# Kernel tuning notes

Measured on AMD Instinct MI355X. Metric: run time of the kernel, lower is better.

Reference implementation:

```python
import jax, jax.numpy as jnp
import numpy as np

B, LQ, LK, D = 4, 256, 256, 768


def setup_inputs() -> dict:
    key = jax.random.key(0)
    ks = jax.random.split(key, 11)
    s = 1.0 / np.sqrt(D)
    return {
        "query": jax.random.normal(ks[0], (B, LQ, D), jnp.float32),
        "key": jax.random.normal(ks[1], (B, LK, D), jnp.float32),
        "value": jax.random.normal(ks[2], (B, LK, D), jnp.float32),
        "Wq": jax.random.uniform(ks[3], (D, D), jnp.float32, -s, s),
        "bq": jax.random.uniform(ks[4], (D,), jnp.float32, -s, s),
        "Wk": jax.random.uniform(ks[5], (D, D), jnp.float32, -s, s),
        "bk": jax.random.uniform(ks[6], (D,), jnp.float32, -s, s),
        "Wv": jax.random.uniform(ks[7], (D, D), jnp.float32, -s, s),
        "bv": jax.random.uniform(ks[8], (D,), jnp.float32, -s, s),
        "Ws": jax.random.uniform(ks[9], (D,), jnp.float32, -s, s),
        "bs": jax.random.uniform(ks[10], (), jnp.float32, -s, s),
    }


def reference(query, key, value, Wq, bq, Wk, bk, Wv, bv, Ws, bs):
    # Linear projections (torch Linear: x @ W.T + b; here W stored as [in, out])
    q = jnp.einsum('bqd,de->bqe', query, Wq) + bq   # [B,Lq,D]
    k = jnp.einsum('bkd,de->bke', key, Wk) + bk     # [B,Lk,D]
    v = jnp.einsum('bkd,de->bke', value, Wv) + bv   # [B,Lk,D]
    # Additive (Bahdanau) scores: tanh(q_i + k_j) . Ws + bs  -> [B,Lq,Lk]
    h = jnp.tanh(q[:, :, None, :] + k[:, None, :, :])  # [B,Lq,Lk,D]
    scores = jnp.einsum('bqkd,d->bqk', h, Ws) + bs
    attention_weights = jax.nn.softmax(scores, axis=-1)  # [B,Lq,Lk]
    attended = jnp.einsum('bqk,bkd->bqd', attention_weights, v)
    return attended, attention_weights
```

## Files before the change

### kernel.cpp

```cpp
#include <hip/hip_runtime.h>

#define NB 4
#define SLQ 256
#define SLK 256
#define DD 768

#define TWO_LOG2E 2.8853900817779268f
#define LOG2E 1.4426950408889634f

typedef _Float16 f16x4 __attribute__((ext_vector_type(4)));
typedef _Float16 f16x8 __attribute__((ext_vector_type(8)));
typedef float f32x4 __attribute__((ext_vector_type(4)));

__device__ __forceinline__ float fexp2(float x) { return __builtin_amdgcn_exp2f(x); }
__device__ __forceinline__ float frcp(float x) { return __builtin_amdgcn_rcpf(x); }

#define LSTR 40

__global__ __launch_bounds__(256) void qkv_f16_kernel(
    const float* __restrict__ query, const float* __restrict__ key_in,
    const float* __restrict__ value, const float* __restrict__ Wq,
    const float* __restrict__ bq, const float* __restrict__ Wk,
    const float* __restrict__ bk, const float* __restrict__ Wv,
    const float* __restrict__ bv, float* __restrict__ eq,
    _Float16* __restrict__ ekh, _Float16* __restrict__ vsh)
{
    const int z = blockIdx.z;
    const float* A = (z == 0) ? query : (z == 1) ? key_in : value;
    const float* W = (z == 0) ? Wq : (z == 1) ? Wk : Wv;
    const float* bias = (z == 0) ? bq : (z == 1) ? bk : bv;

    __shared__ _Float16 Ah[64 * LSTR];
    __shared__ _Float16 Bt[64 * LSTR];

    const int tid = threadIdx.x;
    const int lane = tid & 63;
    const int wid = tid >> 6;
    const int wr = wid >> 1;
    const int wc = wid & 1;
    const int row0 = blockIdx.y * 64;
    const int col0 = blockIdx.x * 64;

    const int ar = tid >> 3;
    const int ac4 = (tid & 7) << 2;
    const int bk_ = tid >> 4;
    const int bn4 = (tid & 15) << 2;

    float4 pa0, pa1, pb0, pb1;
    {
        pa0 = *(const float4*)&A[(size_t)(row0 + ar) * DD + ac4];
        pa1 = *(const float4*)&A[(size_t)(row0 + ar + 32) * DD + ac4];
        pb0 = *(const float4*)&W[(size_t)bk_ * DD + col0 + bn4];
        pb1 = *(const float4*)&W[(size_t)(bk_ + 16) * DD + col0 + bn4];
    }

    f32x4 acc[2][2] = {};
    const int kj = (lane >> 4) << 3;
    const int fr = lane & 15;

    for (int s = 0; s < DD / 32; ++s) {
        __syncthreads();
        {
            f16x4 h;
            h[0] = (_Float16)pa0.x; h[1] = (_Float16)pa0.y;
            h[2] = (_Float16)pa0.z; h[3] = (_Float16)pa0.w;
            *(f16x4*)&Ah[ar * LSTR + ac4] = h;
            h[0] = (_Float16)pa1.x; h[1] = (_Float16)pa1.y;
            h[2] = (_Float16)pa1.z; h[3] = (_Float16)pa1.w;
            *(f16x4*)&Ah[(ar + 32) * LSTR + ac4] = h;
            Bt[(bn4 + 0) * LSTR + bk_] = (_Float16)pb0.x;
            Bt[(bn4 + 1) * LSTR + bk_] = (_Float16)pb0.y;
            Bt[(bn4 + 2) * LSTR + bk_] = (_Float16)pb0.z;
            Bt[(bn4 + 3) * LSTR + bk_] = (_Float16)pb0.w;
            Bt[(bn4 + 0) * LSTR + bk_ + 16] = (_Float16)pb1.x;
            Bt[(bn4 + 1) * LSTR + bk_ + 16] = (_Float16)pb1.y;
            Bt[(bn4 + 2) * LSTR + bk_ + 16] = (_Float16)pb1.z;
            Bt[(bn4 + 3) * LSTR + bk_ + 16] = (_Float16)pb1.w;
        }
        __syncthreads();
        if (s + 1 < DD / 32) {
            const int ks = (s + 1) * 32;
            pa0 = *(const float4*)&A[(size_t)(row0 + ar) * DD + ks + ac4];
            pa1 = *(const float4*)&A[(size_t)(row0 + ar + 32) * DD + ks + ac4];
            pb0 = *(const float4*)&W[(size_t)(ks + bk_) * DD + col0 + bn4];
            pb1 = *(const float4*)&W[(size_t)(ks + bk_ + 16) * DD + col0 + bn4];
        }
        f16x8 af0 = *(const f16x8*)&Ah[(wr * 32 + fr) * LSTR + kj];
        f16x8 af1 = *(const f16x8*)&Ah[(wr * 32 + 16 + fr) * LSTR + kj];
        f16x8 bf0 = *(const f16x8*)&Bt[(wc * 32 + fr) * LSTR + kj];
        f16x8 bf1 = *(const f16x8*)&Bt[(wc * 32 + 16 + fr) * LSTR + kj];
        acc[0][0] = __builtin_amdgcn_mfma_f32_16x16x32_f16(af0, bf0, acc[0][0], 0, 0, 0);
        acc[0][1] = __builtin_amdgcn_mfma_f32_16x16x32_f16(af0, bf1, acc[0][1], 0, 0, 0);
        acc[1][0] = __builtin_amdgcn_mfma_f32_16x16x32_f16(af1, bf0, acc[1][0], 0, 0, 0);
        acc[1][1] = __builtin_amdgcn_mfma_f32_16x16x32_f16(af1, bf1, acc[1][1], 0, 0, 0);
    }

    const int colb = col0 + wc * 32 + fr;
    const int rowb = row0 + wr * 32 + ((lane >> 4) << 2);
#pragma unroll
    for (int mf = 0; mf < 2; ++mf) {
#pragma unroll
        for (int nf = 0; nf < 2; ++nf) {
            const int col = colb + nf * 16;
            const float bv = bias[col];
#pragma unroll
            for (int r = 0; r < 4; ++r) {
                const int row = rowb + mf * 16 + r;
                const float val = acc[mf][nf][r] + bv;
                if (z == 0) {
                    eq[(size_t)row * DD + col] = fexp2(fminf(val * TWO_LOG2E, 15.0f));
                } else if (z == 1) {
                    ekh[(size_t)row * DD + col] =
                        (_Float16)fexp2(fminf(val * TWO_LOG2E, 15.0f));
                } else {
                    vsh[(size_t)row * DD + col] = (_Float16)val;
                }
            }
        }
    }
}

__global__ __launch_bounds__(256) void scores_kernel(
    const float* __restrict__ Eq, const _Float16* __restrict__ Ekh,
    const float* __restrict__ Ws, float* __restrict__ logits)
{
    const int b = blockIdx.z;
    const int k0 = blockIdx.x * 64;
    const int q0 = blockIdx.y * 8;
    const int lane = threadIdx.x & 63;
    const int wid = __builtin_amdgcn_readfirstlane((int)(threadIdx.x >> 6));
    const int q = q0 + (wid << 1);

    const _Float16* kr = Ekh + (size_t)(b * SLK + k0 + lane) * DD;
    const float* qp0 = Eq + (size_t)(b * SLQ + q) * DD;
    const float* qp1 = qp0 + DD;

    float acc0 = 0.f, acc1 = 0.f;

    f16x4 e[4], en[4];
    float g0[16], g1[16], w[16], g0n[16], g1n[16], wn[16];
#pragma unroll
    for (int j = 0; j < 4; ++j) e[j] = *(const f16x4*)(kr + j * 4);
#pragma unroll
    for (int j = 0; j < 16; ++j) { g0[j] = qp0[j]; g1[j] = qp1[j]; w[j] = Ws[j]; }

    for (int c = 0; c < DD / 16; ++c) {
        const int dn = (c + 1) * 16;
        if (c + 1 < DD / 16) {
#pragma unroll
            for (int j = 0; j < 4; ++j) en[j] = *(const f16x4*)(kr + dn + j * 4);
#pragma unroll
            for (int j = 0; j < 16; ++j) {
                g0n[j] = qp0[dn + j]; g1n[j] = qp1[dn + j]; wn[j] = Ws[dn + j];
            }
        }
#pragma unroll
        for (int j = 0; j < 16; ++j) {
            const float ev = (float)e[j >> 2][j & 3];
            const float r0 = frcp(fmaf(g0[j], ev, 1.0f));
            const float r1 = frcp(fmaf(g1[j], ev, 1.0f));
            acc0 = fmaf(w[j], r0, acc0);
            acc1 = fmaf(w[j], r1, acc1);
        }
#pragma unroll
        for (int j = 0; j < 4; ++j) e[j] = en[j];
#pragma unroll
        for (int j = 0; j < 16; ++j) { g0[j] = g0n[j]; g1[j] = g1n[j]; w[j] = wn[j]; }
    }

    logits[(size_t)(b * SLQ + q) * SLK + k0 + lane] = -2.0f * acc0;
    logits[(size_t)(b * SLQ + q + 1) * SLK + k0 + lane] = -2.0f * acc1;
}

__global__ __launch_bounds__(256) void softmax_kernel(float* __restrict__ attn,
                                                      _Float16* __restrict__ phalf)
{
    const int lane = threadIdx.x & 63;
    const int wave = threadIdx.x >> 6;
    const int row = blockIdx.x * 4 + wave;
    float* rp = attn + (size_t)row * SLK;

    float4 x = *(const float4*)&rp[lane << 2];
    float m = fmaxf(fmaxf(x.x, x.y), fmaxf(x.z, x.w));
#pragma unroll
    for (int off = 32; off; off >>= 1) m = fmaxf(m, __shfl_xor(m, off, 64));

    float e0 = fexp2((x.x - m) * LOG2E);
    float e1 = fexp2((x.y - m) * LOG2E);
    float e2 = fexp2((x.z - m) * LOG2E);
    float e3 = fexp2((x.w - m) * LOG2E);
    float s = (e0 + e1) + (e2 + e3);
#pragma unroll
    for (int off = 32; off; off >>= 1) s += __shfl_xor(s, off, 64);

    const float inv = 1.0f / s;
    float4 o;
    o.x = e0 * inv; o.y = e1 * inv; o.z = e2 * inv; o.w = e3 * inv;
    *(float4*)&rp[lane << 2] = o;

    f16x4 h;
    h[0] = (_Float16)o.x; h[1] = (_Float16)o.y;
    h[2] = (_Float16)o.z; h[3] = (_Float16)o.w;
    *(f16x4*)&phalf[(size_t)row * SLK + (lane << 2)] = h;
}

__global__ __launch_bounds__(256) void attended_f16_kernel(
    const _Float16* __restrict__ phalf, const _Float16* __restrict__ vsh,
    float* __restrict__ out)
{
    const int b = blockIdx.z;
    const _Float16* P = phalf + (size_t)b * SLQ * SLK;
    const _Float16* V = vsh + (size_t)b * SLK * DD;
    float* C = out + (size_t)b * SLQ * DD;

    __shared__ _Float16 Ah[64 * LSTR];
    __shared__ _Float16 Bt[64 * LSTR];

    const int tid = threadIdx.x;
    const int lane = tid & 63;
    const int wid = tid >> 6;
    const int wr = wid >> 1;
    const int wc = wid & 1;
    const int row0 = blockIdx.y * 64;
    const int col0 = blockIdx.x * 64;

    const int ar = tid >> 2;
    const int ac8 = (tid & 3) << 3;
    const int bk_ = tid >> 3;
    const int bn8 = (tid & 7) << 3;

    f16x8 pa = *(const f16x8*)&P[(size_t)(row0 + ar) * SLK + ac8];
    f16x8 pb = *(const f16x8*)&V[(size_t)bk_ * DD + col0 + bn8];

    f32x4 acc[2][2] = {};
    const int kj = (lane >> 4) << 3;
    const int fr = lane & 15;

    for (int s = 0; s < SLK / 32; ++s) {
        __syncthreads();
        *(f16x8*)&Ah[ar * LSTR + ac8] = pa;
#pragma unroll
        for (int i = 0; i < 8; ++i) Bt[(bn8 + i) * LSTR + bk_] = pb[i];
        __syncthreads();
        if (s + 1 < SLK / 32) {
            const int ks = (s + 1) * 32;
            pa = *(const f16x8*)&P[(size_t)(row0 + ar) * SLK + ks + ac8];
            pb = *(const f16x8*)&V[(size_t)(ks + bk_) * DD + col0 + bn8];
        }
        f16x8 af0 = *(const f16x8*)&Ah[(wr * 32 + fr) * LSTR + kj];
        f16x8 af1 = *(const f16x8*)&Ah[(wr * 32 + 16 + fr) * LSTR + kj];
        f16x8 bf0 = *(const f16x8*)&Bt[(wc * 32 + fr) * LSTR + kj];
        f16x8 bf1 = *(const f16x8*)&Bt[(wc * 32 + 16 + fr) * LSTR + kj];
        acc[0][0] = __builtin_amdgcn_mfma_f32_16x16x32_f16(af0, bf0, acc[0][0], 0, 0, 0);
        acc[0][1] = __builtin_amdgcn_mfma_f32_16x16x32_f16(af0, bf1, acc[0][1], 0, 0, 0);
        acc[1][0] = __builtin_amdgcn_mfma_f32_16x16x32_f16(af1, bf0, acc[1][0], 0, 0, 0);
        acc[1][1] = __builtin_amdgcn_mfma_f32_16x16x32_f16(af1, bf1, acc[1][1], 0, 0, 0);
    }

    const int colb = col0 + wc * 32 + fr;
    const int rowb = row0 + wr * 32 + ((lane >> 4) << 2);
#pragma unroll
    for (int mf = 0; mf < 2; ++mf)
#pragma unroll
        for (int nf = 0; nf < 2; ++nf)
#pragma unroll
            for (int r = 0; r < 4; ++r)
                C[(size_t)(rowb + mf * 16 + r) * DD + colb + nf * 16] = acc[mf][nf][r];
}

extern "C" void kernel_launch(void* const* d_in, const int* in_sizes, int n_in,
                              void* d_out, int out_size, void* d_ws, size_t ws_size,
                              hipStream_t stream)
{
    (void)in_sizes; (void)n_in; (void)out_size; (void)ws_size;

    const float* query = (const float*)d_in[0];
    const float* key   = (const float*)d_in[1];
    const float* value = (const float*)d_in[2];
    const float* Wq = (const float*)d_in[3];
    const float* bq = (const float*)d_in[4];
    const float* Wk = (const float*)d_in[5];
    const float* bk = (const float*)d_in[6];
    const float* Wv = (const float*)d_in[7];
    const float* bv = (const float*)d_in[8];
    const float* Ws = (const float*)d_in[9];

    const size_t NE = (size_t)NB * SLQ * DD;
    float* eq = (float*)d_ws;
    _Float16* ekh = (_Float16*)(eq + NE);
    _Float16* vsh = ekh + NE;
    _Float16* phalf = vsh + NE;

    float* out = (float*)d_out;
    float* attended = out;
    float* attnw = out + NE;

    qkv_f16_kernel<<<dim3(DD / 64, (NB * SLQ) / 64, 3), 256, 0, stream>>>(
        query, key, value, Wq, bq, Wk, bk, Wv, bv, eq, ekh, vsh);
    scores_kernel<<<dim3(SLK / 64, SLQ / 8, NB), 256, 0, stream>>>(eq, ekh, Ws, attnw);
    softmax_kernel<<<dim3((NB * SLQ) / 4), 256, 0, stream>>>(attnw, phalf);
    attended_f16_kernel<<<dim3(DD / 64, SLQ / 64, NB), 256, 0, stream>>>(phalf, vsh, attended);
}
```

Measured before the change: 157.8 us.

## Pre-convert inputs to fp16, transpose weights/V, fuse scores with softmax

Adds prep kernels that convert Q/K/V activations to fp16 and transpose the projection weights to fp16 [out,in], so the QKV GEMM loads vectorized fp16 rows and skips per-element LDS transposes. V is written transposed so the attended GEMM also loads contiguous rows. Scores and softmax are fused into one kernel with one query row per block, so the fp32 logits are no longer written and reread. This adds two extra launches and extra workspace traffic. The scores kernel now computes one query per thread instead of two, which loses reuse of the K loads.

Result: slower. 174.9 us (+10.8%).

```diff
diff --git a/kernel.cpp b/kernel.cpp
--- a/kernel.cpp
+++ b/kernel.cpp
@@ -17,21 +17,71 @@
 
 #define LSTR 40
 
+__global__ __launch_bounds__(256) void prep_a_kernel(
+    const float* __restrict__ q, const float* __restrict__ k,
+    const float* __restrict__ v, _Float16* __restrict__ qh,
+    _Float16* __restrict__ kh, _Float16* __restrict__ vh)
+{
+    const int z = blockIdx.z;
+    const float* src = (z == 0) ? q : (z == 1) ? k : v;
+    _Float16* dst = (z == 0) ? qh : (z == 1) ? kh : vh;
+    const int i8 = (blockIdx.x * 256 + threadIdx.x) * 8;
+    float4 a = *(const float4*)&src[i8];
+    float4 b = *(const float4*)&src[i8 + 4];
+    f16x8 h;
+    h[0] = (_Float16)a.x; h[1] = (_Float16)a.y; h[2] = (_Float16)a.z; h[3] = (_Float16)a.w;
+    h[4] = (_Float16)b.x; h[5] = (_Float16)b.y; h[6] = (_Float16)b.z; h[7] = (_Float16)b.w;
+    *(f16x8*)&dst[i8] = h;
+}
+
+__global__ __launch_bounds__(256) void prep_wt_kernel(
+    const float* __restrict__ Wq, const float* __restrict__ Wk,
+    const float* __restrict__ Wv, _Float16* __restrict__ wtq,
+    _Float16* __restrict__ wtk, _Float16* __restrict__ wtv)
+{
+    const int z = blockIdx.z;
+    const float* W = (z == 0) ? Wq : (z == 1) ? Wk : Wv;
+    _Float16* Wt = (z == 0) ? wtq : (z == 1) ? wtk : wtv;
+
+    __shared__ float t[64][65];
+    const int tid = threadIdx.x;
+    const int kt0 = blockIdx.y * 64;
+    const int nt0 = blockIdx.x * 64;
+
+    const int col4 = (tid & 15) << 2;
+#pragma unroll
+    for (int i = 0; i < 4; ++i) {
+        const int row = ((tid >> 4) << 2) + i;
+        *(float4*)&t[row][col4] = *(const float4*)&W[(size_t)(kt0 + row) * DD + nt0 + col4];
+    }
+    __syncthreads();
+    const int n = tid >> 2;
+    const int k16 = (tid & 3) << 4;
+    f16x8 h0, h1;
+#pragma unroll
+    for (int j = 0; j < 8; ++j) {
+        h0[j] = (_Float16)t[k16 + j][n];
+        h1[j] = (_Float16)t[k16 + 8 + j][n];
+    }
+    *(f16x8*)&Wt[(size_t)(nt0 + n) * DD + kt0 + k16] = h0;
+    *(f16x8*)&Wt[(size_t)(nt0 + n) * DD + kt0 + k16 + 8] = h1;
+}
+
 __global__ __launch_bounds__(256) void qkv_f16_kernel(
-    const float* __restrict__ query, const float* __restrict__ key_in,
-    const float* __restrict__ value, const float* __restrict__ Wq,
-    const float* __restrict__ bq, const float* __restrict__ Wk,
-    const float* __restrict__ bk, const float* __restrict__ Wv,
+    const _Float16* __restrict__ qh, const _Float16* __restrict__ kh,
+    const _Float16* __restrict__ vh, const _Float16* __restrict__ wtq,
+    const _Float16* __restrict__ wtk, const _Float16* __restrict__ wtv,
+    const float* __restrict__ bq, const float* __restrict__ bk,
     const float* __restrict__ bv, float* __restrict__ eq,
-    _Float16* __restrict__ ekh, _Float16* __restrict__ vsh)
+    _Float16* __restrict__ ekh, _Float16* __restrict__ vsht)
 {
     const int z = blockIdx.z;
-    const float* A = (z == 0) ? query : (z == 1) ? key_in : value;
-    const float* W = (z == 0) ? Wq : (z == 1) ? Wk : Wv;
+    const _Float16* A = (z == 0) ? qh : (z == 1) ? kh : vh;
+    const _Float16* Wt = (z == 0) ? wtq : (z == 1) ? wtk : wtv;
     const float* bias = (z == 0) ? bq : (z == 1) ? bk : bv;
 
     __shared__ _Float16 Ah[64 * LSTR];
-    __shared__ _Float16 Bt[64 * LSTR];
+    __shared__ _Float16 Bh[64 * LSTR];
 
     const int tid = threadIdx.x;
     const int lane = tid & 63;
@@ -41,18 +91,14 @@
     const int row0 = blockIdx.y * 64;
     const int col0 = blockIdx.x * 64;
 
-    const int ar = tid >> 3;
-    const int ac4 = (tid & 7) << 2;
-    const int bk_ = tid >> 4;
-    const int bn4 = (tid & 15) << 2;
-
-    float4 pa0, pa1, pb0, pb1;
-    {
-        pa0 = *(const float4*)&A[(size_t)(row0 + ar) * DD + ac4];
-        pa1 = *(const float4*)&A[(size_t)(row0 + ar + 32) * DD + ac4];
-        pb0 = *(const float4*)&W[(size_t)bk_ * DD + col0 + bn4];
-        pb1 = *(const float4*)&W[(size_t)(bk_ + 16) * DD + col0 + bn4];
-    }
+    const int sr = tid >> 2;
+    const int sc = (tid & 3) << 3;
+
+    const _Float16* Ap = A + (size_t)(row0 + sr) * DD + sc;
+    const _Float16* Bp = Wt + (size_t)(col0 + sr) * DD + sc;
+
+    f16x8 pa = *(const f16x8*)Ap;
+    f16x8 pb = *(const f16x8*)Bp;
 
     f32x4 acc[2][2] = {};
     const int kj = (lane >> 4) << 3;
@@ -60,35 +106,17 @@
 
     for (int s = 0; s < DD / 32; ++s) {
         __syncthreads();
-        {
-            f16x4 h;
-            h[0] = (_Float16)pa0.x; h[1] = (_Float16)pa0.y;
-            h[2] = (_Float16)pa0.z; h[3] = (_Float16)pa0.w;
-            *(f16x4*)&Ah[ar * LSTR + ac4] = h;
-            h[0] = (_Float16)pa1.x; h[1] = (_Float16)pa1.y;
-            h[2] = (_Float16)pa1.z; h[3] = (_Float16)pa1.w;
-            *(f16x4*)&Ah[(ar + 32) * LSTR + ac4] = h;
-            Bt[(bn4 + 0) * LSTR + bk_] = (_Float16)pb0.x;
-            Bt[(bn4 + 1) * LSTR + bk_] = (_Float16)pb0.y;
-            Bt[(bn4 + 2) * LSTR + bk_] = (_Float16)pb0.z;
-            Bt[(bn4 + 3) * LSTR + bk_] = (_Float16)pb0.w;
-            Bt[(bn4 + 0) * LSTR + bk_ + 16] = (_Float16)pb1.x;
-            Bt[(bn4 + 1) * LSTR + bk_ + 16] = (_Float16)pb1.y;
-            Bt[(bn4 + 2) * LSTR + bk_ + 16] = (_Float16)pb1.z;
-            Bt[(bn4 + 3) * LSTR + bk_ + 16] = (_Float16)pb1.w;
-        }
+        *(f16x8*)&Ah[sr * LSTR + sc] = pa;
+        *(f16x8*)&Bh[sr * LSTR + sc] = pb;
         __syncthreads();
         if (s + 1 < DD / 32) {
-            const int ks = (s + 1) * 32;
-            pa0 = *(const float4*)&A[(size_t)(row0 + ar) * DD + ks + ac4];
-            pa1 = *(const float4*)&A[(size_t)(row0 + ar + 32) * DD + ks + ac4];
-            pb0 = *(const float4*)&W[(size_t)(ks + bk_) * DD + col0 + bn4];
-            pb1 = *(const float4*)&W[(size_t)(ks + bk_ + 16) * DD + col0 + bn4];
+            pa = *(const f16x8*)(Ap + (s + 1) * 32);
+            pb = *(const f16x8*)(Bp + (s + 1) * 32);
         }
         f16x8 af0 = *(const f16x8*)&Ah[(wr * 32 + fr) * LSTR + kj];
         f16x8 af1 = *(const f16x8*)&Ah[(wr * 32 + 16 + fr) * LSTR + kj];
-        f16x8 bf0 = *(const f16x8*)&Bt[(wc * 32 + fr) * LSTR + kj];
-        f16x8 bf1 = *(const f16x8*)&Bt[(wc * 32 + 16 + fr) * LSTR + kj];
+        f16x8 bf0 = *(const f16x8*)&Bh[(wc * 32 + fr) * LSTR + kj];
+        f16x8 bf1 = *(const f16x8*)&Bh[(wc * 32 + 16 + fr) * LSTR + kj];
         acc[0][0] = __builtin_amdgcn_mfma_f32_16x16x32_f16(af0, bf0, acc[0][0], 0, 0, 0);
         acc[0][1] = __builtin_amdgcn_mfma_f32_16x16x32_f16(af0, bf1, acc[0][1], 0, 0, 0);
         acc[1][0] = __builtin_amdgcn_mfma_f32_16x16x32_f16(af1, bf0, acc[1][0], 0, 0, 0);
@@ -102,119 +130,103 @@
 #pragma unroll
         for (int nf = 0; nf < 2; ++nf) {
             const int col = colb + nf * 16;
-            const float bv = bias[col];
+            const float bvv = bias[col];
 #pragma unroll
             for (int r = 0; r < 4; ++r) {
                 const int row = rowb + mf * 16 + r;
-                const float val = acc[mf][nf][r] + bv;
+                const float val = acc[mf][nf][r] + bvv;
                 if (z == 0) {
                     eq[(size_t)row * DD + col] = fexp2(fminf(val * TWO_LOG2E, 15.0f));
                 } else if (z == 1) {
                     ekh[(size_t)row * DD + col] =
                         (_Float16)fexp2(fminf(val * TWO_LOG2E, 15.0f));
                 } else {
-                    vsh[(size_t)row * DD + col] = (_Float16)val;
+                    vsht[((size_t)(row >> 8) * DD + col) * SLK + (row & 255)] =
+                        (_Float16)val;
                 }
             }
         }
     }
 }
 
-__global__ __launch_bounds__(256) void scores_kernel(
+__global__ __launch_bounds__(256) void scores_softmax_kernel(
     const float* __restrict__ Eq, const _Float16* __restrict__ Ekh,
-    const float* __restrict__ Ws, float* __restrict__ logits)
-{
-    const int b = blockIdx.z;
-    const int k0 = blockIdx.x * 64;
-    const int q0 = blockIdx.y * 8;
-    const int lane = threadIdx.x & 63;
-    const int wid = __builtin_amdgcn_readfirstlane((int)(threadIdx.x >> 6));
-    const int q = q0 + (wid << 1);
-
-    const _Float16* kr = Ekh + (size_t)(b * SLK + k0 + lane) * DD;
-    const float* qp0 = Eq + (size_t)(b * SLQ + q) * DD;
-    const float* qp1 = qp0 + DD;
-
-    float acc0 = 0.f, acc1 = 0.f;
-
-    f16x4 e[4], en[4];
-    float g0[16], g1[16], w[16], g0n[16], g1n[16], wn[16];
-#pragma unroll
-    for (int j = 0; j < 4; ++j) e[j] = *(const f16x4*)(kr + j * 4);
-#pragma unroll
-    for (int j = 0; j < 16; ++j) { g0[j] = qp0[j]; g1[j] = qp1[j]; w[j] = Ws[j]; }
+    const float* __restrict__ Ws, float* __restrict__ attnw,
+    _Float16* __restrict__ phalf)
+{
+    const int qrow = blockIdx.x;
+    const int b = blockIdx.y;
+    const int tid = threadIdx.x;
+    const int lane = tid & 63;
+    const int w = tid >> 6;
+
+    const _Float16* kr = Ekh + (size_t)(b * SLK + tid) * DD;
+    const float* qp = Eq + (size_t)(b * SLQ + qrow) * DD;
+
+    float acc0 = 0.f, acc1 = 0.f, acc2 = 0.f, acc3 = 0.f;
+
+    f16x8 e0 = *(const f16x8*)kr;
+    f16x8 e1 = *(const f16x8*)(kr + 8);
+    float g[16], wv[16], gn[16], wn[16];
+#pragma unroll
+    for (int j = 0; j < 16; ++j) { g[j] = qp[j]; wv[j] = Ws[j]; }
 
     for (int c = 0; c < DD / 16; ++c) {
+        f16x8 en0, en1;
         const int dn = (c + 1) * 16;
         if (c + 1 < DD / 16) {
-#pragma unroll
-            for (int j = 0; j < 4; ++j) en[j] = *(const f16x4*)(kr + dn + j * 4);
-#pragma unroll
-            for (int j = 0; j < 16; ++j) {
-                g0n[j] = qp0[dn + j]; g1n[j] = qp1[dn + j]; wn[j] = Ws[dn + j];
-            }
-        }
-#pragma unroll
-        for (int j = 0; j < 16; ++j) {
-            const float ev = (float)e[j >> 2][j & 3];
-            const float r0 = frcp(fmaf(g0[j], ev, 1.0f));
-            const float r1 = frcp(fmaf(g1[j], ev, 1.0f));
-            acc0 = fmaf(w[j], r0, acc0);
-            acc1 = fmaf(w[j], r1, acc1);
-        }
-#pragma unroll
-        for (int j = 0; j < 4; ++j) e[j] = en[j];
-#pragma unroll
-        for (int j = 0; j < 16; ++j) { g0[j] = g0n[j]; g1[j] = g1n[j]; w[j] = wn[j]; }
-    }
-
-    logits[(size_t)(b * SLQ + q) * SLK + k0 + lane] = -2.0f * acc0;
-    logits[(size_t)(b * SLQ + q + 1) * SLK + k0 + lane] = -2.0f * acc1;
-}
-
-__global__ __launch_bounds__(256) void softmax_kernel(float* __restrict__ attn,
-                                                      _Float16* __restrict__ phalf)
-{
-    const int lane = threadIdx.x & 63;
-    const int wave = threadIdx.x >> 6;
-    const int row = blockIdx.x * 4 + wave;
-    float* rp = attn + (size_t)row * SLK;
-
-    float4 x = *(const float4*)&rp[lane << 2];
-    float m = fmaxf(fmaxf(x.x, x.y), fmaxf(x.z, x.w));
+            en0 = *(const f16x8*)(kr + dn);
+            en1 = *(const f16x8*)(kr + dn + 8);
+#pragma unroll
+            for (int j = 0; j < 16; ++j) { gn[j] = qp[dn + j]; wn[j] = Ws[dn + j]; }
+        }
+#pragma unroll
+        for (int j = 0; j < 8; ++j) {
+            const float ea = (float)e0[j];
+            const float eb = (float)e1[j];
+            acc0 = fmaf(wv[j], frcp(fmaf(g[j], ea, 1.0f)), acc0);
+            acc1 = fmaf(wv[j + 8], frcp(fmaf(g[j + 8], eb, 1.0f)), acc1);
+        }
+        e0 = en0; e1 = en1;
+#pragma unroll
+        for (int j = 0; j < 16; ++j) { g[j] = gn[j]; wv[j] = wn[j]; }
+    }
+
+    const float logit = -2.0f * ((acc0 + acc1) + (acc2 + acc3));
+
+    __shared__ float redm[4], reds[4];
+    float m = logit;
 #pragma unroll
     for (int off = 32; off; off >>= 1) m = fmaxf(m, __shfl_xor(m, off, 64));
-
-    float e0 = fexp2((x.x - m) * LOG2E);
-    float e1 = fexp2((x.y - m) * LOG2E);
-    float e2 = fexp2((x.z - m) * LOG2E);
-    float e3 = fexp2((x.w - m) * LOG2E);
-    float s = (e0 + e1) + (e2 + e3);
+    if (lane == 0) redm[w] = m;
+    __syncthreads();
+    m = fmaxf(fmaxf(redm[0], redm[1]), fmaxf(redm[2], redm[3]));
+
+    const float ex = fexp2((logit - m) * LOG2E);
+    float s = ex;
 #pragma unroll
     for (int off = 32; off; off >>= 1) s += __shfl_xor(s, off, 64);
-
-    const float inv = 1.0f / s;
-    float4 o;
-    o.x = e0 * inv; o.y = e1 * inv; o.z = e2 * inv; o.w = e3 * inv;
-    *(float4*)&rp[lane << 2] = o;
-
-    f16x4 h;
-    h[0] = (_Float16)o.x; h[1] = (_Float16)o.y;
-    h[2] = (_Float16)o.z; h[3] = (_Float16)o.w;
-    *(f16x4*)&phalf[(size_t)row * SLK + (lane << 2)] = h;
+    if (lane == 0) reds[w] = s;
+    __syncthreads();
+    s = (reds[0] + reds[1]) + (reds[2] + reds[3]);
+
+    const float p = ex * (1.0f / s);
+    const size_t o = (size_t)(b * SLQ + qrow) * SLK + tid;
+    attnw[o] = p;
+    phalf[o] = (_Float16)p;
 }
 
 __global__ __launch_bounds__(256) void attended_f16_kernel(
-    const _Float16* __restrict__ phalf, const _Float16* __restrict__ vsh,
+    const _Float16* __restrict__ phalf, const _Float16* __restrict__ vsht,
     float* __restrict__ out)
 {
     const int b = blockIdx.z;
-    const _Float16* P = phalf + (size_t)b * SLQ * SLK;
-    const _Float16* V = vsh + (size_t)b * SLK * DD;
+    const _Float16* A = phalf + (size_t)b * SLQ * SLK;
+    const _Float16* Bt = vsht + (size_t)b * DD * SLK;
     float* C = out + (size_t)b * SLQ * DD;
 
     __shared__ _Float16 Ah[64 * LSTR];
-    __shared__ _Float16 Bt[64 * LSTR];
+    __shared__ _Float16 Bh[64 * LSTR];
 
     const int tid = threadIdx.x;
     const int lane = tid & 63;
@@ -224,13 +236,14 @@
     const int row0 = blockIdx.y * 64;
     const int col0 = blockIdx.x * 64;
 
-    const int ar = tid >> 2;
-    const int ac8 = (tid & 3) << 3;
-    const int bk_ = tid >> 3;
-    const int bn8 = (tid & 7) << 3;
-
-    f16x8 pa = *(const f16x8*)&P[(size_t)(row0 + ar) * SLK + ac8];
-    f16x8 pb = *(const f16x8*)&V[(size_t)bk_ * DD + col0 + bn8];
+    const int sr = tid >> 2;
+    const int sc = (tid & 3) << 3;
+
+    const _Float16* Ap = A + (size_t)(row0 + sr) * SLK + sc;
+    const _Float16* Bp = Bt + (size_t)(col0 + sr) * SLK + sc;
+
+    f16x8 pa = *(const f16x8*)Ap;
+    f16x8 pb = *(const f16x8*)Bp;
 
     f32x4 acc[2][2] = {};
     const int kj = (lane >> 4) << 3;
@@ -238,19 +251,17 @@
 
     for (int s = 0; s < SLK / 32; ++s) {
         __syncthreads();
-        *(f16x8*)&Ah[ar * LSTR + ac8] = pa;
-#pragma unroll
-        for (int i = 0; i < 8; ++i) Bt[(bn8 + i) * LSTR + bk_] = pb[i];
+        *(f16x8*)&Ah[sr * LSTR + sc] = pa;
+        *(f16x8*)&Bh[sr * LSTR + sc] = pb;
         __syncthreads();
         if (s + 1 < SLK / 32) {
-            const int ks = (s + 1) * 32;
-            pa = *(const f16x8*)&P[(size_t)(row0 + ar) * SLK + ks + ac8];
-            pb = *(const f16x8*)&V[(size_t)(ks + bk_) * DD + col0 + bn8];
+            pa = *(const f16x8*)(Ap + (s + 1) * 32);
+            pb = *(const f16x8*)(Bp + (s + 1) * 32);
         }
         f16x8 af0 = *(const f16x8*)&Ah[(wr * 32 + fr) * LSTR + kj];
         f16x8 af1 = *(const f16x8*)&Ah[(wr * 32 + 16 + fr) * LSTR + kj];
-        f16x8 bf0 = *(const f16x8*)&Bt[(wc * 32 + fr) * LSTR + kj];
-        f16x8 bf1 = *(const f16x8*)&Bt[(wc * 32 + 16 + fr) * LSTR + kj];
+        f16x8 bf0 = *(const f16x8*)&Bh[(wc * 32 + fr) * LSTR + kj];
+        f16x8 bf1 = *(const f16x8*)&Bh[(wc * 32 + 16 + fr) * LSTR + kj];
         acc[0][0] = __builtin_amdgcn_mfma_f32_16x16x32_f16(af0, bf0, acc[0][0], 0, 0, 0);
         acc[0][1] = __builtin_amdgcn_mfma_f32_16x16x32_f16(af0, bf1, acc[0][1], 0, 0, 0);
         acc[1][0] = __builtin_amdgcn_mfma_f32_16x16x32_f16(af1, bf0, acc[1][0], 0, 0, 0);
@@ -286,18 +297,31 @@
     const float* Ws = (const float*)d_in[9];
 
     const size_t NE = (size_t)NB * SLQ * DD;
-    float* eq = (float*)d_ws;
-    _Float16* ekh = (_Float16*)(eq + NE);
-    _Float16* vsh = ekh + NE;
-    _Float16* phalf = vsh + NE;
+    const size_t NW = (size_t)DD * DD;
+
+    char* w = (char*)d_ws;
+    float* eq = (float*)w;               w += NE * 4;
+    _Float16* ekh = (_Float16*)w;        w += NE * 2;
+    _Float16* vsht = (_Float16*)w;       w += NE * 2;
+    _Float16* phalf = (_Float16*)w;      w += (size_t)NB * SLQ * SLK * 2;
+    _Float16* qh = (_Float16*)w;         w += NE * 2;
+    _Float16* kh = (_Float16*)w;         w += NE * 2;
+    _Float16* vh = (_Float16*)w;         w += NE * 2;
+    _Float16* wtq = (_Float16*)w;        w += NW * 2;
+    _Float16* wtk = (_Float16*)w;        w += NW * 2;
+    _Float16* wtv = (_Float16*)w;
 
     float* out = (float*)d_out;
     float* attended = out;
     float* attnw = out + NE;
 
+    prep_a_kernel<<<dim3(NE / (256 * 8), 1, 3), 256, 0, stream>>>(
+        query, key, value, qh, kh, vh);
+    prep_wt_kernel<<<dim3(DD / 64, DD / 64, 3), 256, 0, stream>>>(
+        Wq, Wk, Wv, wtq, wtk, wtv);
     qkv_f16_kernel<<<dim3(DD / 64, (NB * SLQ) / 64, 3), 256, 0, stream>>>(
-        query, key, value, Wq, bq, Wk, bk, Wv, bv, eq, ekh, vsh);
-    scores_kernel<<<dim3(SLK / 64, SLQ / 8, NB), 256, 0, stream>>>(eq, ekh, Ws, attnw);
-    softmax_kernel<<<dim3((NB * SLQ) / 4), 256, 0, stream>>>(attnw, phalf);
-    attended_f16_kernel<<<dim3(DD / 64, SLQ / 64, NB), 256, 0, stream>>>(phalf, vsh, attended);
-}
+        qh, kh, vh, wtq, wtk, wtv, bq, bk, bv, eq, ekh, vsht);
+    scores_softmax_kernel<<<dim3(SLQ, NB), 256, 0, stream>>>(eq, ekh, Ws, attnw, phalf);
+    attended_f16_kernel<<<dim3(DD / 64, SLQ / 64, NB), 256, 0, stream>>>(
+        phalf, vsht, attended);
+}
```
